# Kernel tuning notes

Measured on AMD Instinct MI355X. Metric: run time of the kernel, lower is better.

## Reference

```python
import jax, jax.numpy as jnp
import numpy as np

H = 16      # n_heads
DK = 64     # d_k = d_v = input_dim // n_heads
D = 1024    # input_dim = ouput_dim


def setup_inputs() -> dict:
    key = jax.random.key(0)
    ks = jax.random.split(key, 10)
    s = 1.0 / np.float32(np.sqrt(D))
    inp = {
        'X':  jax.random.normal(ks[0], (2048, D), jnp.float32),
        'X1': jax.random.normal(ks[1], (3072, D), jnp.float32),
        'WQ':  jax.random.normal(ks[2], (D, H * DK), jnp.float32) * s,
        'WK':  jax.random.normal(ks[3], (D, H * DK), jnp.float32) * s,
        'WV':  jax.random.normal(ks[4], (D, H * DK), jnp.float32) * s,
        'WQ1': jax.random.normal(ks[5], (D, H * DK), jnp.float32) * s,
        'WK1': jax.random.normal(ks[6], (D, H * DK), jnp.float32) * s,
        'WV1': jax.random.normal(ks[7], (D, H * DK), jnp.float32) * s,
        'Wfc':  jax.random.normal(ks[8], (H * DK, D), jnp.float32) * s,
        'Wfc1': jax.random.normal(ks[9], (H * DK, D), jnp.float32) * s,
    }
    return inp


def _heads(x):
    # [N, H*DK] -> [H, N, DK]  (matches .view(-1,H,DK).transpose(0,1))
    return x.reshape(-1, H, DK).transpose(1, 0, 2)


def reference(X, X1, WQ, WK, WV, WQ1, WK1, WV1, Wfc, Wfc1):
    scale = jnp.float32(1.0 / np.sqrt(DK))
    Q,  K,  V  = _heads(X @ WQ),  _heads(X @ WK),  _heads(X @ WV)   # [H,N,DK]
    Q1, K1, V1 = _heads(X1 @ WQ1), _heads(X1 @ WK1), _heads(X1 @ WV1)  # [H,N1,DK]

    # direction 1: queries from X1 attend over X
    scores = jnp.einsum('hqd,hkd->hqk', Q1, K) * scale           # [H,N1,N]
    attn = jax.nn.softmax(scores, axis=-1)
    context = jnp.einsum('hqk,hkd->hqd', attn, V)                # [H,N1,DK]

    # direction 2: queries from X attend over X1
    scores1 = jnp.einsum('hqd,hkd->hqk', Q, K1) * scale          # [H,N,N1]
    attn1 = jax.nn.softmax(scores1, axis=-1)
    context1 = jnp.einsum('hqk,hkd->hqd', attn1, V1)             # [H,N,DK]

    # faithful to torch: .transpose(1,2).reshape(-1, H*DK) (head/len axes interleaved)
    context = context.transpose(0, 2, 1).reshape(-1, H * DK)     # [N1, H*DK] rows
    context1 = context1.transpose(0, 2, 1).reshape(-1, H * DK)   # [N,  H*DK] rows

    output = context @ Wfc     # [N1, D]
    output1 = context1 @ Wfc1  # [N,  D]
    return (output, output1)
```

## Files before the change

### kernel.cpp

```cpp
#include <hip/hip_runtime.h>
#include <stdint.h>

typedef unsigned short u16;
typedef unsigned int u32;
typedef u16   u16x4  __attribute__((ext_vector_type(4)));
typedef u16   u16x8  __attribute__((ext_vector_type(8)));
typedef __bf16 bf16x8 __attribute__((ext_vector_type(8)));
typedef float f32x4  __attribute__((ext_vector_type(4)));
typedef u32   u32x2  __attribute__((ext_vector_type(2)));
typedef u32   u32x4  __attribute__((ext_vector_type(4)));

typedef __attribute__((address_space(3))) u16 lds_u16;
typedef __attribute__((address_space(1))) const u16 glb_u16;

static __device__ __forceinline__ u16 f32_bf16(float f) {
    uint32_t u = __builtin_bit_cast(uint32_t, f);
    u += 0x7fffu + ((u >> 16) & 1u);
    return (u16)(u >> 16);
}
static __device__ __forceinline__ u32 pack2(float a, float b) {
#if __has_builtin(__builtin_amdgcn_perm)
    u32 ua = __builtin_bit_cast(u32, a) + 0x8000u;
    u32 ub = __builtin_bit_cast(u32, b) + 0x8000u;
    return __builtin_amdgcn_perm(ub, ua, 0x07060302u);
#else
    return (u32)f32_bf16(a) | ((u32)f32_bf16(b) << 16);
#endif
}
#if __has_builtin(__builtin_amdgcn_exp2f)
#define EXP2(x) __builtin_amdgcn_exp2f(x)
#else
#define EXP2(x) __expf((x) * 0.69314718056f)
#endif
static __device__ __forceinline__ u16x8 cvt8(f32x4 a, f32x4 b) {
    u16x8 v;
#pragma unroll
    for (int e = 0; e < 4; ++e) { v[e] = f32_bf16(a[e]); v[4 + e] = f32_bf16(b[e]); }
    return v;
}

__global__ __launch_bounds__(256) void detect_k(const u16* __restrict__ X, uint32_t* flag) {
    __shared__ int cnt[256];
    int t = threadIdx.x;
    int c = 0;
#pragma unroll
    for (int i = 0; i < 4; ++i) {
        u16 v = X[t + 256 * i];
        int e = (v >> 7) & 0xFF;
        c += (e >= 0xC2) ? 1 : 0;
    }
    cnt[t] = c;
    __syncthreads();
    for (int s = 128; s > 0; s >>= 1) {
        if (t < s) cnt[t] += cnt[t + s];
        __syncthreads();
    }
    if (t == 0) *flag = (cnt[0] > 32) ? 1u : 0u;
}

struct XJob { const void* in; u16* out; int n; };

__global__ __launch_bounds__(256) void convert_x(XJob j0, XJob j1, const uint32_t* __restrict__ flag) {
    const XJob job = (blockIdx.y == 0) ? j0 : j1;
    const bool f32in = (*flag != 0u);
    const int stride = gridDim.x * 256 * 8;
    for (int i = ((int)blockIdx.x * 256 + (int)threadIdx.x) * 8; i < job.n; i += stride) {
        u16x8 v;
        if (f32in) {
            const float* p = (const float*)job.in + i;
            v = cvt8(*(const f32x4*)p, *(const f32x4*)(p + 4));
        } else {
            v = *(const u16x8*)((const u16*)job.in + i);
        }
        *(u16x8*)(job.out + i) = v;
    }
}

struct WJob { const void* in; u16* out; };
struct WBatch8 { WJob j[8]; };

__global__ __launch_bounds__(256) void convert_w(WBatch8 args, const uint32_t* __restrict__ flag) {
    __shared__ u16 tile[64][72];
    const bool f32in = (*flag != 0u);
    const void* in = args.j[blockIdx.z].in;
    u16*       out = args.j[blockIdx.z].out;
    const int t  = threadIdx.x;
    const int r0 = blockIdx.y * 64, c0 = blockIdx.x * 64;
    const int lr = t >> 3, lc = (t & 7) * 8;
#pragma unroll
    for (int pass = 0; pass < 2; ++pass) {
        int r = lr + pass * 32;
        u16x8 v;
        if (f32in) {
            const float* p = (const float*)in + (size_t)(r0 + r) * 1024 + c0 + lc;
            v = cvt8(*(const f32x4*)p, *(const f32x4*)(p + 4));
        } else {
            v = *(const u16x8*)((const u16*)in + (size_t)(r0 + r) * 1024 + c0 + lc);
        }
#pragma unroll
        for (int e = 0; e < 8; ++e) tile[r][lc + e] = v[e];
    }
    __syncthreads();
#pragma unroll
    for (int pass = 0; pass < 2; ++pass) {
        int n = lr + pass * 32;
        u16x8 v;
#pragma unroll
        for (int e = 0; e < 8; ++e) v[e] = tile[lc + e][n];
        *(u16x8*)(out + (size_t)(c0 + n) * 1024 + r0 + lc) = v;
    }
}

struct GemmJob  { const u16* A; const u16* Bt; void* C; int M; int cF32able; int cOffElems; int vtNk; float cScale; };
struct GemmBatch6 { GemmJob j[6]; };

__global__ __launch_bounds__(256) void gemm_bt(GemmBatch6 b, const uint32_t* __restrict__ flag) {
    const GemmJob job = b.j[blockIdx.z];
    const int K = 1024, N = 1024;
    const int m0 = blockIdx.x * 128;
    if (m0 >= job.M) return;
    const int n0 = blockIdx.y * 128;
    const bool cF = job.cF32able && (*flag != 0u);

    __shared__ u16 As[128 * 64];
    __shared__ u16 Bs[128 * 64];

    const int tid  = threadIdx.x;
    const int lane = tid & 63, wave = tid >> 6;
    const int quad = lane >> 4, l16 = lane & 15;
    const int wrow = wave >> 1, wcol = wave & 1;

    f32x4 acc[4][4];
#pragma unroll
    for (int i = 0; i < 4; ++i)
#pragma unroll
        for (int j = 0; j < 4; ++j) acc[i][j] = (f32x4){0.f, 0.f, 0.f, 0.f};

    for (int k0 = 0; k0 < K; k0 += 64) {
        __syncthreads();
#pragma unroll
        for (int i = 0; i < 4; ++i) {
            int id = tid + 256 * i;
            int row = id >> 3, slot = id & 7;
            int src = (slot ^ (row & 7)) * 8;
            __builtin_amdgcn_global_load_lds(
                (glb_u16*)(job.A + (size_t)(m0 + row) * K + k0 + src),
                (lds_u16*)(As + (size_t)id * 8), 16, 0, 0);
            __builtin_amdgcn_global_load_lds(
                (glb_u16*)(job.Bt + (size_t)(n0 + row) * K + k0 + src),
                (lds_u16*)(Bs + (size_t)id * 8), 16, 0, 0);
        }
        __syncthreads();

#pragma unroll
        for (int kc2 = 0; kc2 < 2; ++kc2) {
            bf16x8 af[4], bfb[4];
#pragma unroll
            for (int i = 0; i < 4; ++i) {
                int r  = wrow * 64 + i * 16 + l16;
                af[i]  = *(const bf16x8*)(As + r * 64 + (((kc2 * 4 + quad) ^ (r & 7)) * 8));
                int rn = wcol * 64 + i * 16 + l16;
                bfb[i] = *(const bf16x8*)(Bs + rn * 64 + (((kc2 * 4 + quad) ^ (rn & 7)) * 8));
            }
#pragma unroll
            for (int i = 0; i < 4; ++i)
#pragma unroll
                for (int j = 0; j < 4; ++j)
                    acc[i][j] = __builtin_amdgcn_mfma_f32_16x16x32_bf16(af[i], bfb[j], acc[i][j], 0, 0, 0);
        }
    }

    if (job.vtNk > 0) {
        u16* VT = (u16*)job.C;
        const int Nk2 = job.vtNk;
#pragma unroll
        for (int i = 0; i < 4; ++i)
#pragma unroll
            for (int j = 0; j < 4; ++j) {
                int n   = n0 + wcol * 64 + j * 16 + l16;
                int hh  = n >> 6, dd = n & 63;
                int key = m0 + wrow * 64 + i * 16 + quad * 4;
                int bq  = key & 31;
                int kp  = (key & ~31) | (((bq >> 2) & 3) * 8 + (bq >> 4) * 4);
                u16x4 vv;
#pragma unroll
                for (int r = 0; r < 4; ++r) vv[r] = f32_bf16(acc[i][j][r]);
                *(u16x4*)(VT + (size_t)hh * 64 * Nk2 + (size_t)dd * Nk2 + kp) = vv;
            }
    } else if (cF) {
        float* C = (float*)job.C + job.cOffElems;
#pragma unroll
        for (int i = 0; i < 4; ++i)
#pragma unroll
            for (int j = 0; j < 4; ++j)
#pragma unroll
                for (int r = 0; r < 4; ++r) {
                    int gr = m0 + wrow * 64 + i * 16 + quad * 4 + r;
                    int gc = n0 + wcol * 64 + j * 16 + l16;
                    C[(size_t)gr * N + gc] = acc[i][j][r];
                }
    } else {
        u16* C = (u16*)job.C + job.cOffElems;
        const float cs = job.cScale;
#pragma unroll
        for (int i = 0; i < 4; ++i)
#pragma unroll
            for (int j = 0; j < 4; ++j)
#pragma unroll
                for (int r = 0; r < 4; ++r) {
                    int gr = m0 + wrow * 64 + i * 16 + quad * 4 + r;
                    int gc = n0 + wcol * 64 + j * 16 + l16;
                    C[(size_t)gr * N + gc] = f32_bf16(acc[i][j][r] * cs);
                }
    }
}

struct AttnDir { const u16* Q; const u16* K; const u16* VT; u16* ctxT; int Nq; int Nk; int nBlk; };

__global__ __launch_bounds__(256, 8) void attn_k(AttnDir d0, AttnDir d1) {
    const int D = 1024;
    int b = blockIdx.x;
    const AttnDir dd = (b < d0.nBlk) ? d0 : d1;
    if (blockIdx.x >= (unsigned)d0.nBlk) b -= d0.nBlk;
    const int h  = b & 15;
    const int q0 = (b >> 4) * 64;
    const int Nq = dd.Nq, Nk = dd.Nk;
    const u16* __restrict__ Qp  = dd.Q;
    const u16* __restrict__ Kp  = dd.K;
    const u16* __restrict__ VTp = dd.VT;

    const int tid  = threadIdx.x;
    const int lane = tid & 63, w = tid >> 6;
    const int quad = lane >> 4, l16 = lane & 15;

    __shared__ u16 smem[2][4096];

    bf16x8 aq[2];
#pragma unroll
    for (int kc = 0; kc < 2; ++kc) {
        int q = q0 + w * 16 + l16;
        aq[kc] = *(const bf16x8*)(Qp + (size_t)q * D + h * 64 + kc * 32 + quad * 8);
    }

    f32x4 o[4];
#pragma unroll
    for (int nj = 0; nj < 4; ++nj) o[nj] = (f32x4){0.f, 0.f, 0.f, 0.f};
    float rs = 0.f;

    const int krow = tid >> 3;
    const int ksrc = ((tid & 7) ^ (krow & 7)) * 8;
    const u16* kg = Kp + (size_t)krow * D + h * 64 + ksrc;
    const u16* vg = VTp + (size_t)h * 64 * Nk + (size_t)(tid >> 2) * Nk + (tid & 3) * 8;

    const int nt = Nk >> 5;
    __builtin_amdgcn_global_load_lds((glb_u16*)kg, (lds_u16*)(&smem[0][0] + tid * 8), 16, 0, 0);
    __builtin_amdgcn_global_load_lds((glb_u16*)vg, (lds_u16*)(&smem[0][2048] + tid * 8), 16, 0, 0);
    kg += (size_t)32 * D; vg += 32;
    __syncthreads();

    for (int t = 0; t < nt; ++t) {
        const u16* Ks = &smem[t & 1][0];
        const u16* Vs = Ks + 2048;
        if (t + 1 < nt) {
            u16* dst = &smem[(t + 1) & 1][0];
            __builtin_amdgcn_global_load_lds((glb_u16*)kg, (lds_u16*)(dst + tid * 8), 16, 0, 0);
            __builtin_amdgcn_global_load_lds((glb_u16*)vg, (lds_u16*)(dst + 2048 + tid * 8), 16, 0, 0);
            kg += (size_t)32 * D; vg += 32;
        }

        f32x4 s[2];
#pragma unroll
        for (int kn = 0; kn < 2; ++kn) s[kn] = (f32x4){0.f, 0.f, 0.f, 0.f};
#pragma unroll
        for (int kn = 0; kn < 2; ++kn)
#pragma unroll
            for (int kc = 0; kc < 2; ++kc) {
                int keyr = kn * 16 + l16;
                int phys = ((kc * 4 + quad) ^ (keyr & 7)) * 8;
                bf16x8 ak = *(const bf16x8*)(Ks + keyr * 64 + phys);
                s[kn] = __builtin_amdgcn_mfma_f32_16x16x32_bf16(ak, aq[kc], s[kn], 0, 0, 0);
            }

        u32x4 pbf;
#pragma unroll
        for (int kn = 0; kn < 2; ++kn) {
            float p0 = EXP2(s[kn][0]);
            float p1 = EXP2(s[kn][1]);
            float p2 = EXP2(s[kn][2]);
            float p3 = EXP2(s[kn][3]);
            rs += (p0 + p1) + (p2 + p3);
            pbf[kn * 2 + 0] = pack2(p0, p1);
            pbf[kn * 2 + 1] = pack2(p2, p3);
        }

#pragma unroll
        for (int nj = 0; nj < 4; ++nj) {
            int d = nj * 16 + l16;
            bf16x8 va = *(const bf16x8*)(Vs + d * 32 + quad * 8);
            o[nj] = __builtin_amdgcn_mfma_f32_16x16x32_bf16(
                va, __builtin_bit_cast(bf16x8, pbf), o[nj], 0, 0, 0);
        }

        __syncthreads();
    }

    rs += __shfl_xor(rs, 16, 64);
    rs += __shfl_xor(rs, 32, 64);
    const float inv = 1.0f / rs;
    const int q = q0 + w * 16 + l16;
#pragma unroll
    for (int nj = 0; nj < 4; ++nj)
#pragma unroll
        for (int r = 0; r < 4; ++r) {
            int d = nj * 16 + quad * 4 + r;
            dd.ctxT[(size_t)(h * 64 + d) * Nq + q] = f32_bf16(o[nj][r] * inv);
        }
}

extern "C" void kernel_launch(void* const* d_in, const int* in_sizes, int n_in,
                              void* d_out, int out_size, void* d_ws, size_t ws_size,
                              hipStream_t stream) {
    u16* ws = (u16*)d_ws;
    uint32_t* flag = (uint32_t*)ws;
    u16* A = ws + 64;
    const size_t M1 = 1024ull * 1024;
    const float QSC = 0.125f * 1.44269504089f;

    u16* W8   = A;
    u16* Kd1  = A + 8 * M1;
    u16* VT   = A + 10 * M1;
    u16* K1d  = A + 12 * M1;
    u16* VT1  = A + 15 * M1;
    u16* ctx2 = A + 18 * M1;

    u16* outw = (u16*)d_out;
    u16* Q1s  = outw;
    u16* Qs   = outw + 3 * M1;
    u16* Xb   = outw + 5 * M1;
    u16* X1b  = outw + 7 * M1;

    u16* ctx1 = W8;
    u16* WfcT = W8 + 6 * M1;

    detect_k<<<dim3(1), dim3(256), 0, stream>>>((const u16*)d_in[0], flag);

    XJob xj0 = {d_in[0], Xb,  2048 * 1024};
    XJob xj1 = {d_in[1], X1b, 3072 * 1024};
    convert_x<<<dim3(128, 2), dim3(256), 0, stream>>>(xj0, xj1, flag);

    WBatch8 wb;
    for (int i = 0; i < 8; ++i) { wb.j[i].in = d_in[2 + i]; wb.j[i].out = W8 + (size_t)i * M1; }
    convert_w<<<dim3(16, 16, 8), dim3(256), 0, stream>>>(wb, flag);

    GemmBatch6 gp;
    gp.j[0] = (GemmJob){Xb,  W8,          Qs,  2048, 0, 0, 0,    QSC};
    gp.j[1] = (GemmJob){Xb,  W8 + M1,     Kd1, 2048, 0, 0, 0,    1.0f};
    gp.j[2] = (GemmJob){Xb,  W8 + 2 * M1, VT,  2048, 0, 0, 2048, 1.0f};
    gp.j[3] = (GemmJob){X1b, W8 + 3 * M1, Q1s, 3072, 0, 0, 0,    QSC};
    gp.j[4] = (GemmJob){X1b, W8 + 4 * M1, K1d, 3072, 0, 0, 0,    1.0f};
    gp.j[5] = (GemmJob){X1b, W8 + 5 * M1, VT1, 3072, 0, 0, 3072, 1.0f};
    gemm_bt<<<dim3(24, 8, 6), dim3(256), 0, stream>>>(gp, flag);

    AttnDir a0 = {Qs,  K1d, VT1, ctx2, 2048, 3072, 512};
    AttnDir a1 = {Q1s, Kd1, VT,  ctx1, 3072, 2048, 768};
    attn_k<<<dim3(1280), dim3(256), 0, stream>>>(a0, a1);

    GemmBatch6 gf;
    gf.j[0] = (GemmJob){ctx1, WfcT,      d_out, 3072, 1, 0,               0, 1.0f};
    gf.j[1] = (GemmJob){ctx2, WfcT + M1, d_out, 2048, 1, 3 * 1024 * 1024, 0, 1.0f};
    gf.j[2] = gf.j[0]; gf.j[3] = gf.j[0]; gf.j[4] = gf.j[0]; gf.j[5] = gf.j[0];
    gemm_bt<<<dim3(24, 8, 2), dim3(256), 0, stream>>>(gf, flag);
}
```

Measured before the change: 255.4 us.

## Fuse dtype detection and conversions into one launch, compact GEMM grids

Removes the separate detect kernel by having every block of the conversion and final GEMM kernels recompute the input-dtype flag with a block reduction. It merges the X and weight conversion kernels into one launch and replaces the 3D GEMM grids, which held many early-exit blocks, with compact 1D grids mapped to exact tile counts. The aim is to cut launch count and idle blocks, at the cost of redundant per-block flag reductions and extra syncs.

```diff
diff --git a/kernel.cpp b/kernel.cpp
--- a/kernel.cpp
+++ b/kernel.cpp
@@ -39,13 +39,13 @@
     return v;
 }
 
-__global__ __launch_bounds__(256) void detect_k(const u16* __restrict__ X, uint32_t* flag) {
-    __shared__ int cnt[256];
-    int t = threadIdx.x;
+static __device__ __forceinline__ bool flag_reduce(const u16* __restrict__ X0,
+                                                   int* cnt ) {
+    const int t = threadIdx.x;
     int c = 0;
 #pragma unroll
     for (int i = 0; i < 4; ++i) {
-        u16 v = X[t + 256 * i];
+        u16 v = X0[t + 256 * i];
         int e = (v >> 7) & 0xFF;
         c += (e >= 0xC2) ? 1 : 0;
     }
@@ -55,37 +55,41 @@
         if (t < s) cnt[t] += cnt[t + s];
         __syncthreads();
     }
-    if (t == 0) *flag = (cnt[0] > 32) ? 1u : 0u;
+    bool f = cnt[0] > 32;
+    __syncthreads();
+    return f;
 }
 
 struct XJob { const void* in; u16* out; int n; };
-
-__global__ __launch_bounds__(256) void convert_x(XJob j0, XJob j1, const uint32_t* __restrict__ flag) {
-    const XJob job = (blockIdx.y == 0) ? j0 : j1;
-    const bool f32in = (*flag != 0u);
-    const int stride = gridDim.x * 256 * 8;
-    for (int i = ((int)blockIdx.x * 256 + (int)threadIdx.x) * 8; i < job.n; i += stride) {
-        u16x8 v;
-        if (f32in) {
-            const float* p = (const float*)job.in + i;
-            v = cvt8(*(const f32x4*)p, *(const f32x4*)(p + 4));
-        } else {
-            v = *(const u16x8*)((const u16*)job.in + i);
-        }
-        *(u16x8*)(job.out + i) = v;
-    }
-}
-
 struct WJob { const void* in; u16* out; };
 struct WBatch8 { WJob j[8]; };
 
-__global__ __launch_bounds__(256) void convert_w(WBatch8 args, const uint32_t* __restrict__ flag) {
+__global__ __launch_bounds__(256) void convert_all(XJob j0, XJob j1, WBatch8 args) {
+    __shared__ int cnt[256];
     __shared__ u16 tile[64][72];
-    const bool f32in = (*flag != 0u);
-    const void* in = args.j[blockIdx.z].in;
-    u16*       out = args.j[blockIdx.z].out;
-    const int t  = threadIdx.x;
-    const int r0 = blockIdx.y * 64, c0 = blockIdx.x * 64;
+    const bool f32in = flag_reduce((const u16*)j0.in, cnt);
+    const int t = threadIdx.x;
+
+    if (blockIdx.y < 2) {
+        const XJob job = (blockIdx.y == 0) ? j0 : j1;
+        const int stride = gridDim.x * 256 * 8;
+        for (int i = ((int)blockIdx.x * 256 + t) * 8; i < job.n; i += stride) {
+            u16x8 v;
+            if (f32in) {
+                const float* p = (const float*)job.in + i;
+                v = cvt8(*(const f32x4*)p, *(const f32x4*)(p + 4));
+            } else {
+                v = *(const u16x8*)((const u16*)job.in + i);
+            }
+            *(u16x8*)(job.out + i) = v;
+        }
+        return;
+    }
+
+    const int wj = blockIdx.y - 2;
+    const void* in = args.j[wj].in;
+    u16*       out = args.j[wj].out;
+    const int r0 = ((int)blockIdx.x >> 4) * 64, c0 = ((int)blockIdx.x & 15) * 64;
     const int lr = t >> 3, lc = (t & 7) * 8;
 #pragma unroll
     for (int pass = 0; pass < 2; ++pass) {
@@ -112,18 +116,32 @@
 }
 
 struct GemmJob  { const u16* A; const u16* Bt; void* C; int M; int cF32able; int cOffElems; int vtNk; float cScale; };
-struct GemmBatch6 { GemmJob j[6]; };
-
-__global__ __launch_bounds__(256) void gemm_bt(GemmBatch6 b, const uint32_t* __restrict__ flag) {
-    const GemmJob job = b.j[blockIdx.z];
+struct GemmBatch6 { GemmJob j[6]; const u16* flagSrc; int mode; };
+
+__global__ __launch_bounds__(256) void gemm_bt(GemmBatch6 b) {
     const int K = 1024, N = 1024;
-    const int m0 = blockIdx.x * 128;
+    int jz, m_t, n_t;
+    {
+        int bid = blockIdx.x;
+        if (b.mode == 1) {
+            if (bid < 576) { jz = 3 + bid / 192; int r = bid % 192; m_t = r % 24; n_t = r / 24; }
+            else { int b2 = bid - 576; jz = b2 / 128; int r = b2 % 128; m_t = r % 16; n_t = r / 16; }
+        } else {
+            if (bid < 192) { jz = 0; m_t = bid % 24; n_t = bid / 24; }
+            else { int b2 = bid - 192; jz = 1; m_t = b2 % 16; n_t = b2 / 16; }
+        }
+    }
+    const GemmJob job = b.j[jz];
+    const int m0 = m_t * 128, n0 = n_t * 128;
     if (m0 >= job.M) return;
-    const int n0 = blockIdx.y * 128;
-    const bool cF = job.cF32able && (*flag != 0u);
 
     __shared__ u16 As[128 * 64];
     __shared__ u16 Bs[128 * 64];
+
+    bool cF = false;
+    if (b.mode == 2 && job.cF32able) {
+        cF = flag_reduce(b.flagSrc, (int*)As);
+    }
 
     const int tid  = threadIdx.x;
     const int lane = tid & 63, wave = tid >> 6;
@@ -321,7 +339,6 @@
                               void* d_out, int out_size, void* d_ws, size_t ws_size,
                               hipStream_t stream) {
     u16* ws = (u16*)d_ws;
-    uint32_t* flag = (uint32_t*)ws;
     u16* A = ws + 64;
     const size_t M1 = 1024ull * 1024;
     const float QSC = 0.125f * 1.44269504089f;
@@ -342,15 +359,11 @@
     u16* ctx1 = W8;
     u16* WfcT = W8 + 6 * M1;
 
-    detect_k<<<dim3(1), dim3(256), 0, stream>>>((const u16*)d_in[0], flag);
-
     XJob xj0 = {d_in[0], Xb,  2048 * 1024};
     XJob xj1 = {d_in[1], X1b, 3072 * 1024};
-    convert_x<<<dim3(128, 2), dim3(256), 0, stream>>>(xj0, xj1, flag);
-
     WBatch8 wb;
     for (int i = 0; i < 8; ++i) { wb.j[i].in = d_in[2 + i]; wb.j[i].out = W8 + (size_t)i * M1; }
-    convert_w<<<dim3(16, 16, 8), dim3(256), 0, stream>>>(wb, flag);
+    convert_all<<<dim3(256, 10), dim3(256), 0, stream>>>(xj0, xj1, wb);
 
     GemmBatch6 gp;
     gp.j[0] = (GemmJob){Xb,  W8,          Qs,  2048, 0, 0, 0,    QSC};
@@ -359,7 +372,9 @@
     gp.j[3] = (GemmJob){X1b, W8 + 3 * M1, Q1s, 3072, 0, 0, 0,    QSC};
     gp.j[4] = (GemmJob){X1b, W8 + 4 * M1, K1d, 3072, 0, 0, 0,    1.0f};
     gp.j[5] = (GemmJob){X1b, W8 + 5 * M1, VT1, 3072, 0, 0, 3072, 1.0f};
-    gemm_bt<<<dim3(24, 8, 6), dim3(256), 0, stream>>>(gp, flag);
+    gp.flagSrc = (const u16*)d_in[0];
+    gp.mode = 1;
+    gemm_bt<<<dim3(960), dim3(256), 0, stream>>>(gp);
 
     AttnDir a0 = {Qs,  K1d, VT1, ctx2, 2048, 3072, 512};
     AttnDir a1 = {Q1s, Kd1, VT,  ctx1, 3072, 2048, 768};
@@ -369,5 +384,7 @@
     gf.j[0] = (GemmJob){ctx1, WfcT,      d_out, 3072, 1, 0,               0, 1.0f};
     gf.j[1] = (GemmJob){ctx2, WfcT + M1, d_out, 2048, 1, 3 * 1024 * 1024, 0, 1.0f};
     gf.j[2] = gf.j[0]; gf.j[3] = gf.j[0]; gf.j[4] = gf.j[0]; gf.j[5] = gf.j[0];
-    gemm_bt<<<dim3(24, 8, 2), dim3(256), 0, stream>>>(gf, flag);
-}
+    gf.flagSrc = (const u16*)d_in[0];
+    gf.mode = 2;
+    gemm_bt<<<dim3(320), dim3(256), 0, stream>>>(gf);
+}
```

Result: faster. 247.4 us (-3.1%).
